# Kernel optimization log

Measured on AMD Instinct MI355X. Metric: run time of the kernel, lower is better.

Reference implementation:

```python
import jax, jax.numpy as jnp
import numpy as np

B, SQ, SK, D = 32, 2048, 2048, 64


def setup_inputs() -> dict:
    key = jax.random.key(0)
    kq, kk, km = jax.random.split(key, 3)
    q = jax.random.normal(kq, (B, SQ, D), dtype=jnp.float32)
    k = jax.random.normal(kk, (B, SK, D), dtype=jnp.float32)
    mask = jax.random.randint(km, (B, SQ, SK), 0, 2, dtype=jnp.int32)
    return {"q": q, "k": k, "mask": mask}


def reference(q, k, mask):
    # scores = q @ k^T / sqrt(D)  -> [B, SQ, SK]
    scale = 1.0 / np.sqrt(q.shape[-1]).astype(np.float32)
    scores = jnp.einsum('bqd,bkd->bqk', q, k) * scale
    scores = jnp.where(mask == 0, -jnp.inf, scores)
    return jax.nn.softmax(scores, axis=-1)
```

## Files before the change

### kernel.cpp

```cpp
#include <hip/hip_runtime.h>
#include <math.h>

constexpr int BB  = 32;
constexpr int SQL = 2048;
constexpr int SKL = 2048;
constexpr int DD  = 64;

using f32x4 = __attribute__((ext_vector_type(4))) float;
using bfrag = __attribute__((ext_vector_type(8))) short;
typedef unsigned long long u64;

static __device__ __forceinline__ unsigned short f2bf(float x) {
    unsigned u = __float_as_uint(x);
    u = u + 0x7FFFu + ((u >> 16) & 1u);
    return (unsigned short)(u >> 16);
}
static __device__ __forceinline__ float bf2f(unsigned short h) {
    return __uint_as_float((unsigned)h << 16);
}

static __device__ __forceinline__ void gld16(const void* g, void* l) {
    __builtin_amdgcn_global_load_lds(
        (const __attribute__((address_space(1))) void*)(size_t)g,
        (__attribute__((address_space(3))) void*)(unsigned)(size_t)l,
        16, 0, 0);
}

__global__ __launch_bounds__(256) void split_k_swz(
    const float* __restrict__ k, unsigned char* __restrict__ kswz)
{
    const int i0 = blockIdx.x * blockDim.x + threadIdx.x;
    const int g  = i0 & 7;
    const int c  = (i0 >> 3) & 2047;
    const int b  = i0 >> 14;
    const float* kp = k + ((size_t)(b * 2048 + c)) * DD + g * 8;
    bfrag h, lo;
    #pragma unroll
    for (int j = 0; j < 8; ++j) {
        const float x = kp[j];
        const unsigned short hh = f2bf(x);
        h[j]  = (short)hh;
        lo[j] = (short)f2bf(x - bf2f(hh));
    }
    const int sw = (c & 7) << 4;
    unsigned char* rec = kswz + ((size_t)(b * 2048 + c)) * 256;
    *(bfrag*)(rec + ((g * 16) ^ sw))       = h;
    *(bfrag*)(rec + 128 + ((g * 16) ^ sw)) = lo;
}

#define MF(A, B, C) __builtin_amdgcn_mfma_f32_16x16x32_bf16((A), (B), (C), 0, 0, 0)

template<bool PRE>
__global__ __launch_bounds__(512, 4) void sdpa_v18(
    const float* __restrict__ q, const float* __restrict__ k,
    const int* __restrict__ mask, const unsigned char* __restrict__ kswz,
    float* __restrict__ out)
{
    __shared__ char kring[8][2][4096];
    __shared__ u64  bitlds[16][32];

    const int t   = threadIdx.x;
    const int l   = t & 63;
    const int w   = t >> 6;
    const int lr  = l & 15;
    const int lg  = l >> 4;
    const int bid = blockIdx.x;
    const int swz = (bid & 7) * 512 + (bid >> 3);
    const int b   = swz >> 7;
    const int r0  = (swz & 127) * 16;
    const int c0  = w * 256;
    const size_t rowg = (size_t)b * SQL + (size_t)(r0 + lr);
    const int swk = (lr & 7) << 4;

    {
        const int crow = t >> 5;
        const int cseg = t & 31;
        const int* mrow = mask + ((size_t)b * SQL + (size_t)(r0 + crow)) * SKL
                               + cseg * 64;
        u64 bits = 0;
        #pragma unroll
        for (int j = 0; j < 16; ++j) {
            const int4 v = *(const int4*)(mrow + j * 4);
            bits |= (u64)(v.x != 0 ? 1u : 0u) << (j * 4 + 0);
            bits |= (u64)(v.y != 0 ? 1u : 0u) << (j * 4 + 1);
            bits |= (u64)(v.z != 0 ? 1u : 0u) << (j * 4 + 2);
            bits |= (u64)(v.w != 0 ? 1u : 0u) << (j * 4 + 3);
        }
        bitlds[crow][cseg] = bits;
    }

    constexpr float QS = 0.18033688011112042f;
    bfrag qh0, ql0, qh1, ql1;
    {
        const float* qp = q + rowg * DD + lg * 8;
        const f32x4 x0 = *(const f32x4*)qp;
        const f32x4 x1 = *(const f32x4*)(qp + 4);
        const f32x4 y0 = *(const f32x4*)(qp + 32);
        const f32x4 y1 = *(const f32x4*)(qp + 36);
        #pragma unroll
        for (int j = 0; j < 4; ++j) {
            float a = x0[j] * QS, c = x1[j] * QS;
            float d = y0[j] * QS, e = y1[j] * QS;
            unsigned short h;
            h = f2bf(a); qh0[j]     = (short)h; ql0[j]     = (short)f2bf(a - bf2f(h));
            h = f2bf(c); qh0[j + 4] = (short)h; ql0[j + 4] = (short)f2bf(c - bf2f(h));
            h = f2bf(d); qh1[j]     = (short)h; ql1[j]     = (short)f2bf(d - bf2f(h));
            h = f2bf(e); qh1[j + 4] = (short)h; ql1[j + 4] = (short)f2bf(e - bf2f(h));
        }
    }

    __syncthreads();

    const u64 ma0 = bitlds[lr][w * 4 + 0];
    const u64 ma1 = bitlds[lr][w * 4 + 1];
    const u64 ma2 = bitlds[lr][w * 4 + 2];
    const u64 ma3 = bitlds[lr][w * 4 + 3];

    const char*  ksrc = PRE ? (const char*)(kswz + ((size_t)b * SKL + c0) * 256) : nullptr;
    const float* kraw = PRE ? nullptr : k + (size_t)b * SKL * DD;
    char* kseg = &kring[w][0][0];

#define STAGE(T)                                                               \
    do {                                                                       \
        char* _kd = kseg + (((T) & 1) << 12);                                  \
        if constexpr (PRE) {                                                   \
            const char* _ks = ksrc + (size_t)(T) * 4096;                       \
            gld16(_ks + l * 16,        _kd + l * 16);                          \
            gld16(_ks + 1024 + l * 16, _kd + 1024 + l * 16);                   \
            gld16(_ks + 2048 + l * 16, _kd + 2048 + l * 16);                   \
            gld16(_ks + 3072 + l * 16, _kd + 3072 + l * 16);                   \
        } else {                                                               \
            const float* _kc = kraw + (size_t)(c0 + (T) * 16 + lr) * DD;       \
            const f32x4 _a0 = *(const f32x4*)(_kc + lg * 8);                   \
            const f32x4 _a1 = *(const f32x4*)(_kc + lg * 8 + 4);               \
            const f32x4 _b0 = *(const f32x4*)(_kc + (lg + 4) * 8);             \
            const f32x4 _b1 = *(const f32x4*)(_kc + (lg + 4) * 8 + 4);         \
            bfrag _h, _o;                                                      \
            _Pragma("unroll")                                                  \
            for (int _j = 0; _j < 4; ++_j) {                                   \
                unsigned short _t2;                                            \
                _t2 = f2bf(_a0[_j]); _h[_j]   = (short)_t2;                    \
                _o[_j]   = (short)f2bf(_a0[_j] - bf2f(_t2));                   \
                _t2 = f2bf(_a1[_j]); _h[_j+4] = (short)_t2;                    \
                _o[_j+4] = (short)f2bf(_a1[_j] - bf2f(_t2));                   \
            }                                                                  \
            char* _rec = _kd + lr * 256;                                       \
            *(bfrag*)(_rec + ((lg * 16) ^ swk))       = _h;                    \
            *(bfrag*)(_rec + 128 + ((lg * 16) ^ swk)) = _o;                    \
            _Pragma("unroll")                                                  \
            for (int _j = 0; _j < 4; ++_j) {                                   \
                unsigned short _t2;                                            \
                _t2 = f2bf(_b0[_j]); _h[_j]   = (short)_t2;                    \
                _o[_j]   = (short)f2bf(_b0[_j] - bf2f(_t2));                   \
                _t2 = f2bf(_b1[_j]); _h[_j+4] = (short)_t2;                    \
                _o[_j+4] = (short)f2bf(_b1[_j] - bf2f(_t2));                   \
            }                                                                  \
            *(bfrag*)(_rec + (((lg + 4) * 16) ^ swk))       = _h;              \
            *(bfrag*)(_rec + 128 + (((lg + 4) * 16) ^ swk)) = _o;              \
        }                                                                      \
    } while (0)

    STAGE(0);
    STAGE(1);

    unsigned sc[32];
    float psum = 0.f;

#define ITER(T, VMC, MW)                                                       \
    do {                                                                       \
        if constexpr (PRE)                                                     \
            asm volatile("s_waitcnt vmcnt(" #VMC ")" ::: "memory");            \
        const char* _c = kseg + (((T) & 1) << 12) + lr * 256;                  \
        const bfrag _kh0 = *(const bfrag*)(_c + ((lg * 16) ^ swk));            \
        const bfrag _kh1 = *(const bfrag*)(_c + (((lg + 4) * 16) ^ swk));      \
        const bfrag _kl0 = *(const bfrag*)(_c + 128 + ((lg * 16) ^ swk));      \
        const bfrag _kl1 = *(const bfrag*)(_c + 128 + (((lg + 4) * 16) ^ swk));\
        asm volatile("s_waitcnt lgkmcnt(0)" ::: "memory");                     \
        __builtin_amdgcn_sched_barrier(0);                                     \
        if constexpr ((T) + 2 < 16) STAGE((T) + 2);                            \
                                                   \
        f32x4 _h = {0.f, 0.f, 0.f, 0.f};                                       \
        f32x4 _m = {0.f, 0.f, 0.f, 0.f};                                       \
        _h = MF(_kh0, qh0, _h);  _m = MF(_kh0, ql0, _m);                       \
        _h = MF(_kh1, qh1, _h);  _m = MF(_kl0, qh0, _m);                       \
        _m = MF(_kh1, ql1, _m);  _m = MF(_kl1, qh1, _m);                       \
        const f32x4 _s = _h + _m;                                              \
        const unsigned _n = (unsigned)((MW) >> (((T) & 3) * 16 + lg * 4)) & 0xFu; \
        const float _e0 = (_n & 1u) ? exp2f(_s[0]) : 0.f;                      \
        const float _e1 = (_n & 2u) ? exp2f(_s[1]) : 0.f;                      \
        const float _e2 = (_n & 4u) ? exp2f(_s[2]) : 0.f;                      \
        const float _e3 = (_n & 8u) ? exp2f(_s[3]) : 0.f;                      \
        psum += (_e0 + _e1) + (_e2 + _e3);                                     \
        asm volatile("v_cvt_pk_bf16_f32 %0, %1, %2"                            \
                     : "=v"(sc[2 * (T)])     : "v"(_e0), "v"(_e1));            \
        asm volatile("v_cvt_pk_bf16_f32 %0, %1, %2"                            \
                     : "=v"(sc[2 * (T) + 1]) : "v"(_e2), "v"(_e3));            \
    } while (0)

    ITER(0,  4, ma0); ITER(1,  4, ma0); ITER(2,  4, ma0); ITER(3,  4, ma0);
    ITER(4,  4, ma1); ITER(5,  4, ma1); ITER(6,  4, ma1); ITER(7,  4, ma1);
    ITER(8,  4, ma2); ITER(9,  4, ma2); ITER(10, 4, ma2); ITER(11, 4, ma2);
    ITER(12, 4, ma3); ITER(13, 4, ma3); ITER(14, 4, ma3); ITER(15, 0, ma3);
#undef ITER
#undef STAGE

    psum += __shfl_xor(psum, 16, 64);
    psum += __shfl_xor(psum, 32, 64);

    __syncthreads();
    float* s_red = (float*)&bitlds[0][0];
    if (l < 16) s_red[w * 16 + lr] = psum;
    __syncthreads();

    float tot = 0.f;
    #pragma unroll
    for (int ww = 0; ww < 8; ++ww)
        tot += s_red[ww * 16 + lr];
    const float rinv = 1.0f / tot;

    float* op = out + rowg * SKL + c0 + lg * 4;
    #pragma unroll
    for (int T = 0; T < 16; ++T) {
        const unsigned p01 = sc[2 * T];
        const unsigned p23 = sc[2 * T + 1];
        f32x4 o;
        o[0] = bf2f((unsigned short)(p01 & 0xffffu)) * rinv;
        o[1] = bf2f((unsigned short)(p01 >> 16))     * rinv;
        o[2] = bf2f((unsigned short)(p23 & 0xffffu)) * rinv;
        o[3] = bf2f((unsigned short)(p23 >> 16))     * rinv;
        *reinterpret_cast<f32x4*>(op + T * 16) = o;
    }
}

extern "C" void kernel_launch(void* const* d_in, const int* in_sizes, int n_in,
                              void* d_out, int out_size, void* d_ws, size_t ws_size,
                              hipStream_t stream) {
    const float* q    = (const float*)d_in[0];
    const float* k    = (const float*)d_in[1];
    const int*   mask = (const int*)d_in[2];
    float*       out  = (float*)d_out;

    const size_t KS_B = (size_t)BB * SKL * 256;

    dim3 grid(4096);

    if (ws_size >= KS_B) {
        unsigned char* ksp = (unsigned char*)d_ws;
        split_k_swz<<<2048, 256, 0, stream>>>(k, ksp);
        sdpa_v18<true><<<grid, 512, 0, stream>>>(q, k, mask, ksp, out);
    } else {
        sdpa_v18<false><<<grid, 512, 0, stream>>>(q, k, mask, nullptr, out);
    }
}
```

Before: 322.4 us.

## Precompress mask to bits, drop K low-part split, deepen K prefetch ring

A separate kernel now packs the int32 mask into a bitmask in workspace, so the main kernel reads each row's mask bits straight from global memory. This removes the in-kernel LDS bitmask build and one block barrier. K is now kept as bf16-high only (half the bytes), which drops two of the six MFMAs per tile at some accuracy cost. The LDS ring goes from 2 to 4 slots with a prefetch distance of 3. The extra mask pass still reads the full int32 mask and adds a launch, so total memory traffic may not fall.

```diff
diff --git a/kernel.cpp b/kernel.cpp
--- a/kernel.cpp
+++ b/kernel.cpp
@@ -26,7 +26,29 @@
         16, 0, 0);
 }
 
-__global__ __launch_bounds__(256) void split_k_swz(
+__global__ __launch_bounds__(256) void compress_mask(
+    const int* __restrict__ m, unsigned char* __restrict__ bm)
+{
+    const int t = threadIdx.x;
+    const size_t g0 = (size_t)blockIdx.x * 1024 + t;
+    const int4* mp = (const int4*)m;
+    int4 a0 = mp[(g0)       * 2], a1 = mp[(g0)       * 2 + 1];
+    int4 b0 = mp[(g0 + 256) * 2], b1 = mp[(g0 + 256) * 2 + 1];
+    int4 c0 = mp[(g0 + 512) * 2], c1 = mp[(g0 + 512) * 2 + 1];
+    int4 d0 = mp[(g0 + 768) * 2], d1 = mp[(g0 + 768) * 2 + 1];
+#define PACK8(v0, v1)                                                         \
+    (unsigned char)((v0.x != 0 ? 1u : 0u)  | (v0.y != 0 ? 2u : 0u)   |        \
+                    (v0.z != 0 ? 4u : 0u)  | (v0.w != 0 ? 8u : 0u)   |        \
+                    (v1.x != 0 ? 16u : 0u) | (v1.y != 0 ? 32u : 0u)  |        \
+                    (v1.z != 0 ? 64u : 0u) | (v1.w != 0 ? 128u : 0u))
+    bm[g0]       = PACK8(a0, a1);
+    bm[g0 + 256] = PACK8(b0, b1);
+    bm[g0 + 512] = PACK8(c0, c1);
+    bm[g0 + 768] = PACK8(d0, d1);
+#undef PACK8
+}
+
+__global__ __launch_bounds__(256) void split_k1(
     const float* __restrict__ k, unsigned char* __restrict__ kswz)
 {
     const int i0 = blockIdx.x * blockDim.x + threadIdx.x;
@@ -34,30 +56,26 @@
     const int c  = (i0 >> 3) & 2047;
     const int b  = i0 >> 14;
     const float* kp = k + ((size_t)(b * 2048 + c)) * DD + g * 8;
-    bfrag h, lo;
+    bfrag h;
     #pragma unroll
-    for (int j = 0; j < 8; ++j) {
-        const float x = kp[j];
-        const unsigned short hh = f2bf(x);
-        h[j]  = (short)hh;
-        lo[j] = (short)f2bf(x - bf2f(hh));
-    }
-    const int sw = (c & 7) << 4;
-    unsigned char* rec = kswz + ((size_t)(b * 2048 + c)) * 256;
-    *(bfrag*)(rec + ((g * 16) ^ sw))       = h;
-    *(bfrag*)(rec + 128 + ((g * 16) ^ sw)) = lo;
+    for (int j = 0; j < 8; ++j)
+        h[j] = (short)f2bf(kp[j]);
+    unsigned char* rec = kswz + ((size_t)(b * 2048 + c)) * 128;
+    *(bfrag*)(rec + 16 * (g ^ (c & 7))) = h;
 }
 
 #define MF(A, B, C) __builtin_amdgcn_mfma_f32_16x16x32_bf16((A), (B), (C), 0, 0, 0)
+#define NIB4(M) ((unsigned)((M).x ? 1u:0u) | ((M).y ? 2u:0u) |                 \
+                 ((M).z ? 4u:0u) | ((M).w ? 8u:0u))
 
 template<bool PRE>
-__global__ __launch_bounds__(512, 4) void sdpa_v18(
+__global__ __launch_bounds__(512, 4) void sdpa_v20(
     const float* __restrict__ q, const float* __restrict__ k,
-    const int* __restrict__ mask, const unsigned char* __restrict__ kswz,
-    float* __restrict__ out)
+    const int* __restrict__ mask, const unsigned char* __restrict__ bm,
+    const unsigned char* __restrict__ kswz, float* __restrict__ out)
 {
-    __shared__ char kring[8][2][4096];
-    __shared__ u64  bitlds[16][32];
+    __shared__ char  kring[8][4][2048];
+    __shared__ float s_red[8][16];
 
     const int t   = threadIdx.x;
     const int l   = t & 63;
@@ -70,23 +88,13 @@
     const int r0  = (swz & 127) * 16;
     const int c0  = w * 256;
     const size_t rowg = (size_t)b * SQL + (size_t)(r0 + lr);
-    const int swk = (lr & 7) << 4;
-
-    {
-        const int crow = t >> 5;
-        const int cseg = t & 31;
-        const int* mrow = mask + ((size_t)b * SQL + (size_t)(r0 + crow)) * SKL
-                               + cseg * 64;
-        u64 bits = 0;
-        #pragma unroll
-        for (int j = 0; j < 16; ++j) {
-            const int4 v = *(const int4*)(mrow + j * 4);
-            bits |= (u64)(v.x != 0 ? 1u : 0u) << (j * 4 + 0);
-            bits |= (u64)(v.y != 0 ? 1u : 0u) << (j * 4 + 1);
-            bits |= (u64)(v.z != 0 ? 1u : 0u) << (j * 4 + 2);
-            bits |= (u64)(v.w != 0 ? 1u : 0u) << (j * 4 + 3);
-        }
-        bitlds[crow][cseg] = bits;
+
+    u64 ba0 = 0, ba1 = 0, ba2 = 0, ba3 = 0;
+    if constexpr (PRE) {
+        const ulonglong2* wp = (const ulonglong2*)(bm + rowg * (SKL / 8) + w * 32);
+        const ulonglong2 v0 = wp[0];
+        const ulonglong2 v1 = wp[1];
+        ba0 = v0.x; ba1 = v0.y; ba2 = v1.x; ba3 = v1.y;
     }
 
     constexpr float QS = 0.18033688011112042f;
@@ -108,84 +116,68 @@
             h = f2bf(e); qh1[j + 4] = (short)h; ql1[j + 4] = (short)f2bf(e - bf2f(h));
         }
     }
-
-    __syncthreads();
-
-    const u64 ma0 = bitlds[lr][w * 4 + 0];
-    const u64 ma1 = bitlds[lr][w * 4 + 1];
-    const u64 ma2 = bitlds[lr][w * 4 + 2];
-    const u64 ma3 = bitlds[lr][w * 4 + 3];
-
-    const char*  ksrc = PRE ? (const char*)(kswz + ((size_t)b * SKL + c0) * 256) : nullptr;
+    __builtin_amdgcn_sched_barrier(0);
+
+    const char*  ksrc = PRE ? (const char*)(kswz + ((size_t)b * SKL + c0) * 128) : nullptr;
     const float* kraw = PRE ? nullptr : k + (size_t)b * SKL * DD;
+    const int*   mrp  = PRE ? nullptr : mask + rowg * SKL + c0 + lg * 4;
     char* kseg = &kring[w][0][0];
 
 #define STAGE(T)                                                               \
     do {                                                                       \
-        char* _kd = kseg + (((T) & 1) << 12);                                  \
         if constexpr (PRE) {                                                   \
-            const char* _ks = ksrc + (size_t)(T) * 4096;                       \
+            char* _kd = kseg + (((T) & 3) << 11);                              \
+            const char* _ks = ksrc + (size_t)(T) * 2048;                       \
             gld16(_ks + l * 16,        _kd + l * 16);                          \
             gld16(_ks + 1024 + l * 16, _kd + 1024 + l * 16);                   \
-            gld16(_ks + 2048 + l * 16, _kd + 2048 + l * 16);                   \
-            gld16(_ks + 3072 + l * 16, _kd + 3072 + l * 16);                   \
+        }                                                                      \
+    } while (0)
+
+    STAGE(0);
+    STAGE(1);
+    STAGE(2);
+
+    unsigned sc[32];
+    float psum = 0.f;
+
+#define ITER(T, VMC, MW)                                                       \
+    do {                                                                       \
+        bfrag _kh0, _kh1;                                                      \
+        int4 _mv;                                                              \
+        if constexpr (PRE) {                                                   \
+            asm volatile("s_waitcnt vmcnt(" #VMC ")" ::: "memory");            \
+            const char* _c = kseg + (((T) & 3) << 11) + lr * 128;              \
+            _kh0 = *(const bfrag*)(_c + 16 * (lg ^ (lr & 7)));                 \
+            _kh1 = *(const bfrag*)(_c + 16 * ((4 | lg) ^ (lr & 7)));           \
+            asm volatile("s_waitcnt lgkmcnt(0)" ::: "memory");                 \
+            __builtin_amdgcn_sched_barrier(0);                                 \
+            if constexpr ((T) + 3 < 16) STAGE((T) + 3);                        \
         } else {                                                               \
             const float* _kc = kraw + (size_t)(c0 + (T) * 16 + lr) * DD;       \
-            const f32x4 _a0 = *(const f32x4*)(_kc + lg * 8);                   \
-            const f32x4 _a1 = *(const f32x4*)(_kc + lg * 8 + 4);               \
-            const f32x4 _b0 = *(const f32x4*)(_kc + (lg + 4) * 8);             \
-            const f32x4 _b1 = *(const f32x4*)(_kc + (lg + 4) * 8 + 4);         \
-            bfrag _h, _o;                                                      \
+            const f32x4 _v0 = *(const f32x4*)(_kc + lg * 8);                   \
+            const f32x4 _v1 = *(const f32x4*)(_kc + lg * 8 + 4);               \
+            const f32x4 _v2 = *(const f32x4*)(_kc + 32 + lg * 8);              \
+            const f32x4 _v3 = *(const f32x4*)(_kc + 36 + lg * 8);              \
             _Pragma("unroll")                                                  \
             for (int _j = 0; _j < 4; ++_j) {                                   \
-                unsigned short _t2;                                            \
-                _t2 = f2bf(_a0[_j]); _h[_j]   = (short)_t2;                    \
-                _o[_j]   = (short)f2bf(_a0[_j] - bf2f(_t2));                   \
-                _t2 = f2bf(_a1[_j]); _h[_j+4] = (short)_t2;                    \
-                _o[_j+4] = (short)f2bf(_a1[_j] - bf2f(_t2));                   \
+                _kh0[_j]     = (short)f2bf(_v0[_j]);                           \
+                _kh0[_j + 4] = (short)f2bf(_v1[_j]);                           \
+                _kh1[_j]     = (short)f2bf(_v2[_j]);                           \
+                _kh1[_j + 4] = (short)f2bf(_v3[_j]);                           \
             }                                                                  \
-            char* _rec = _kd + lr * 256;                                       \
-            *(bfrag*)(_rec + ((lg * 16) ^ swk))       = _h;                    \
-            *(bfrag*)(_rec + 128 + ((lg * 16) ^ swk)) = _o;                    \
-            _Pragma("unroll")                                                  \
-            for (int _j = 0; _j < 4; ++_j) {                                   \
-                unsigned short _t2;                                            \
-                _t2 = f2bf(_b0[_j]); _h[_j]   = (short)_t2;                    \
-                _o[_j]   = (short)f2bf(_b0[_j] - bf2f(_t2));                   \
-                _t2 = f2bf(_b1[_j]); _h[_j+4] = (short)_t2;                    \
-                _o[_j+4] = (short)f2bf(_b1[_j] - bf2f(_t2));                   \
-            }                                                                  \
-            *(bfrag*)(_rec + (((lg + 4) * 16) ^ swk))       = _h;              \
-            *(bfrag*)(_rec + 128 + (((lg + 4) * 16) ^ swk)) = _o;              \
+            _mv = *(const int4*)(mrp + (T) * 16);                              \
         }                                                                      \
-    } while (0)
-
-    STAGE(0);
-    STAGE(1);
-
-    unsigned sc[32];
-    float psum = 0.f;
-
-#define ITER(T, VMC, MW)                                                       \
-    do {                                                                       \
-        if constexpr (PRE)                                                     \
-            asm volatile("s_waitcnt vmcnt(" #VMC ")" ::: "memory");            \
-        const char* _c = kseg + (((T) & 1) << 12) + lr * 256;                  \
-        const bfrag _kh0 = *(const bfrag*)(_c + ((lg * 16) ^ swk));            \
-        const bfrag _kh1 = *(const bfrag*)(_c + (((lg + 4) * 16) ^ swk));      \
-        const bfrag _kl0 = *(const bfrag*)(_c + 128 + ((lg * 16) ^ swk));      \
-        const bfrag _kl1 = *(const bfrag*)(_c + 128 + (((lg + 4) * 16) ^ swk));\
-        asm volatile("s_waitcnt lgkmcnt(0)" ::: "memory");                     \
-        __builtin_amdgcn_sched_barrier(0);                                     \
-        if constexpr ((T) + 2 < 16) STAGE((T) + 2);                            \
-                                                   \
+                               \
         f32x4 _h = {0.f, 0.f, 0.f, 0.f};                                       \
         f32x4 _m = {0.f, 0.f, 0.f, 0.f};                                       \
         _h = MF(_kh0, qh0, _h);  _m = MF(_kh0, ql0, _m);                       \
-        _h = MF(_kh1, qh1, _h);  _m = MF(_kl0, qh0, _m);                       \
-        _m = MF(_kh1, ql1, _m);  _m = MF(_kl1, qh1, _m);                       \
+        _h = MF(_kh1, qh1, _h);  _m = MF(_kh1, ql1, _m);                       \
         const f32x4 _s = _h + _m;                                              \
-        const unsigned _n = (unsigned)((MW) >> (((T) & 3) * 16 + lg * 4)) & 0xFu; \
+        unsigned _n;                                                           \
+        if constexpr (PRE)                                                     \
+            _n = (unsigned)((MW) >> (((T) & 3) * 16 + lg * 4)) & 0xFu;         \
+        else                                                                   \
+            _n = NIB4(_mv);                                                    \
         const float _e0 = (_n & 1u) ? exp2f(_s[0]) : 0.f;                      \
         const float _e1 = (_n & 2u) ? exp2f(_s[1]) : 0.f;                      \
         const float _e2 = (_n & 4u) ? exp2f(_s[2]) : 0.f;                      \
@@ -197,25 +189,22 @@
                      : "=v"(sc[2 * (T) + 1]) : "v"(_e2), "v"(_e3));            \
     } while (0)
 
-    ITER(0,  4, ma0); ITER(1,  4, ma0); ITER(2,  4, ma0); ITER(3,  4, ma0);
-    ITER(4,  4, ma1); ITER(5,  4, ma1); ITER(6,  4, ma1); ITER(7,  4, ma1);
-    ITER(8,  4, ma2); ITER(9,  4, ma2); ITER(10, 4, ma2); ITER(11, 4, ma2);
-    ITER(12, 4, ma3); ITER(13, 4, ma3); ITER(14, 4, ma3); ITER(15, 0, ma3);
+    ITER(0,  4, ba0); ITER(1,  4, ba0); ITER(2,  4, ba0); ITER(3,  4, ba0);
+    ITER(4,  4, ba1); ITER(5,  4, ba1); ITER(6,  4, ba1); ITER(7,  4, ba1);
+    ITER(8,  4, ba2); ITER(9,  4, ba2); ITER(10, 4, ba2); ITER(11, 4, ba2);
+    ITER(12, 4, ba3); ITER(13, 4, ba3); ITER(14, 2, ba3); ITER(15, 0, ba3);
 #undef ITER
 #undef STAGE
 
     psum += __shfl_xor(psum, 16, 64);
     psum += __shfl_xor(psum, 32, 64);
-
-    __syncthreads();
-    float* s_red = (float*)&bitlds[0][0];
-    if (l < 16) s_red[w * 16 + lr] = psum;
+    if (l < 16) s_red[w][lr] = psum;
     __syncthreads();
 
     float tot = 0.f;
     #pragma unroll
     for (int ww = 0; ww < 8; ++ww)
-        tot += s_red[ww * 16 + lr];
+        tot += s_red[ww][lr];
     const float rinv = 1.0f / tot;
 
     float* op = out + rowg * SKL + c0 + lg * 4;
@@ -240,15 +229,18 @@
     const int*   mask = (const int*)d_in[2];
     float*       out  = (float*)d_out;
 
-    const size_t KS_B = (size_t)BB * SKL * 256;
+    const size_t BM_B = (size_t)BB * SQL * SKL / 8;
+    const size_t KS_B = (size_t)BB * SKL * 128;
 
     dim3 grid(4096);
 
-    if (ws_size >= KS_B) {
-        unsigned char* ksp = (unsigned char*)d_ws;
-        split_k_swz<<<2048, 256, 0, stream>>>(k, ksp);
-        sdpa_v18<true><<<grid, 512, 0, stream>>>(q, k, mask, ksp, out);
+    if (ws_size >= BM_B + KS_B) {
+        unsigned char* bmp = (unsigned char*)d_ws;
+        unsigned char* ksp = (unsigned char*)d_ws + BM_B;
+        compress_mask<<<16384, 256, 0, stream>>>(mask, bmp);
+        split_k1<<<2048, 256, 0, stream>>>(k, ksp);
+        sdpa_v20<true><<<grid, 512, 0, stream>>>(q, k, mask, bmp, ksp, out);
     } else {
-        sdpa_v18<false><<<grid, 512, 0, stream>>>(q, k, mask, nullptr, out);
-    }
-}
+        sdpa_v20<false><<<grid, 512, 0, stream>>>(q, k, mask, nullptr, nullptr, out);
+    }
+}
```

New measurement: 303.5 us. -5.9%, faster.
